# Kernel tuning notes

Hardware: AMD Instinct MI355X
Metric: run time of the kernel (lower is better)

Reference implementation:

```python
import jax, jax.numpy as jnp
import numpy as np

T, B, C, H, W = 4, 8, 256, 56, 56
HEADS = 8
D_NORM = 8.0
LAMDA = 1
CV = C * LAMDA
EPS = 1e-5


def quant_if(x, D):
    # Q_IFNode with Quant surrogate: integer spike counts clip(round(x),0,D),
    # straight-through gradient = 1 on [0, D].
    y = jnp.clip(jnp.round(x), 0.0, D)
    mask = ((x >= 0.0) & (x <= D)).astype(x.dtype)
    return x * mask + jax.lax.stop_gradient(y - x * mask)


def conv_bn(x, w, p):
    # 1x1 conv (pointwise channel mix) fused with eval-mode BatchNorm.
    # x: [T,B,Cin,H,W], w: [Cout,Cin], p: [4,Cout]=(gamma,beta,mean,var)
    y = jnp.einsum('oc,tbchw->tbohw', w, x)
    gamma, beta, mean, var = p[0], p[1], p[2], p[3]
    s = gamma / jnp.sqrt(var + EPS)
    return y * s[None, None, :, None, None] + (beta - mean * s)[None, None, :, None, None]


def _to_heads(t, c):
    # [T,B,c,H,W] -> [T,B,HEADS,N,c//HEADS]  (channel split h-outer, matches torch reshape)
    return t.reshape(T, B, HEADS, c // HEADS, H * W).transpose(0, 1, 2, 4, 3)


def setup_inputs():
    key = jax.random.key(0)
    ks = jax.random.split(key, 9)

    def bn_params(k, c):
        k1, k2, k3, k4 = jax.random.split(k, 4)
        return jnp.stack([
            jax.random.uniform(k1, (c,)) + 0.5,        # gamma
            jax.random.normal(k2, (c,)) * 0.1,          # beta
            jax.random.normal(k3, (c,)) * 0.1,          # running mean
            jax.random.uniform(k4, (c,)) + 0.5,         # running var
        ]).astype(jnp.float32)

    x = jax.random.normal(ks[0], (T, B, C, H, W), dtype=jnp.float32)
    w_scale = 1.0 / np.sqrt(C)
    return {
        'x': x,
        'qw': jax.random.normal(ks[1], (C, C), dtype=jnp.float32) * w_scale,
        'qbn': bn_params(ks[2], C),
        'kw': jax.random.normal(ks[3], (C, C), dtype=jnp.float32) * w_scale,
        'kbn': bn_params(ks[4], C),
        'vw': jax.random.normal(ks[5], (CV, C), dtype=jnp.float32) * w_scale,
        'vbn': bn_params(ks[6], CV),
        'pw': jax.random.normal(ks[7], (C, CV), dtype=jnp.float32) * w_scale,
        'pbn': bn_params(ks[8], C),
    }


def reference(x, qw, qbn, kw, kbn, vw, vbn, pw, pbn):
    dh = C // HEADS
    scale = dh ** (-0.5)

    xs = quant_if(x, D_NORM) / D_NORM                       # head_spike / D_Norm
    q = conv_bn(xs, qw, qbn)
    k = conv_bn(xs, kw, kbn)
    v = conv_bn(xs, vw, vbn)

    qh = _to_heads(quant_if(q, D_NORM) / D_NORM, C)         # [T,B,h,N,dh]
    kh = _to_heads(quant_if(k, D_NORM) / D_NORM, C)
    vh = _to_heads(quant_if(v, D_NORM) / D_NORM, CV)        # [T,B,h,N,dv]

    # Softmax-free linear attention: (q @ k^T) @ v == q @ (k^T @ v), O(N*d^2).
    kv = jnp.einsum('tbhnd,tbhne->tbhde', kh, vh)            # [T,B,h,dh,dv]
    o = jnp.einsum('tbhnd,tbhde->tbhne', qh, kv) * (scale * 2.0)

    # [T,B,h,N,dv] -> [T,B,CV,N]
    o = o.transpose(0, 1, 2, 4, 3).reshape(T, B, CV, H * W)
    o = quant_if(o, D_NORM) / D_NORM                         # attn_spike / D_Norm
    o = o.reshape(T, B, CV, H, W)
    out = conv_bn(o, pw, pbn)                                # [T,B,C,H,W]
    return out
```

## Files before the change

### kernel.cpp

```cpp
#include <hip/hip_runtime.h>
#include <stdint.h>

#define TB_ 32
#define C_ 256
#define N_ 3136
#define TBC (C_ * N_)
#define ACT_SZ (TB_ * TBC)
#define XSB_TB 819200
#define PARTS 7
#define CHUNK 448

typedef __attribute__((ext_vector_type(8))) short bf16x8;
typedef __attribute__((ext_vector_type(4))) float f32x4;

__device__ __forceinline__ void glds16(const void* gp, void* lp) {
  __builtin_amdgcn_global_load_lds(
      (const __attribute__((address_space(1))) unsigned int*)gp,
      (__attribute__((address_space(3))) unsigned int*)lp, 16, 0, 0);
}

__device__ __forceinline__ unsigned short bf16rn(float f, float* val) {
  unsigned b = __float_as_uint(f);
  unsigned r = (b + 0x7fffu + ((b >> 16) & 1u)) >> 16;
  *val = __uint_as_float(r << 16);
  return (unsigned short)r;
}

__device__ __forceinline__ int dot4u(unsigned a, unsigned b, int c) {
  c += (int)(a & 255u)         * (int)(b & 255u);
  c += (int)((a >> 8) & 255u)  * (int)((b >> 8) & 255u);
  c += (int)((a >> 16) & 255u) * (int)((b >> 16) & 255u);
  c += (int)(a >> 24)          * (int)(b >> 24);
  return c;
}

__device__ __forceinline__ int dot4(unsigned a, unsigned b, int c) {
#if defined(__has_builtin)
#if __has_builtin(__builtin_amdgcn_sdot4)
  return __builtin_amdgcn_sdot4((int)a, (int)b, c, false);
#else
  return dot4u(a, b, c);
#endif
#else
  return dot4u(a, b, c);
#endif
}

__global__ __launch_bounds__(256) void prep_all(
    const float* __restrict__ qbn, const float* __restrict__ kbn,
    const float* __restrict__ vbn, const float* __restrict__ pbn,
    const float* __restrict__ qw, const float* __restrict__ kw,
    const float* __restrict__ vw, const float* __restrict__ pw,
    float* __restrict__ bnw, unsigned short* __restrict__ wsp,
    int* __restrict__ kvg) {
  const int bx = blockIdx.x;
  const int t = threadIdx.x;
  if (bx == 0) {
    const float* ps[4] = {qbn, kbn, vbn, pbn};
#pragma unroll
    for (int i = 0; i < 4; ++i) {
      const float* p = ps[i];
      float g = p[t], be = p[256 + t], mn = p[512 + t], vr = p[768 + t];
      float s = g / sqrtf(vr + 1e-5f);
      float b = __fsub_rn(be, __fmul_rn(mn, s));
      bnw[i * 512 + t] = s;
      bnw[i * 512 + 256 + t] = b;
    }
  } else if (bx <= 1024) {
    const float* Ws[4] = {qw, kw, vw, pw};
    int id = bx - 1, co = id & 255, m = id >> 8;
    float w = Ws[m][co * 256 + t];
    float h1, h2, h3r;
    unsigned short u1 = bf16rn(w, &h1);
    float r1 = __fsub_rn(w, h1);
    unsigned short u2 = bf16rn(r1, &h2);
    float r2 = __fsub_rn(r1, h2);
    unsigned short u3 = bf16rn(r2, &h3r);
    int rt = co >> 7, ks = t >> 5;
    int lane = (co & 15) + 16 * ((t >> 3) & 3);
    unsigned short us[3] = {u1, u2, u3};
#pragma unroll
    for (int sp = 0; sp < 3; ++sp) {
      size_t off = (size_t)((((m * 3 + sp) * 2 + rt) * 8 + ks)) * 4096 + lane * 8 + (t & 7);
      wsp[off] = us[sp];
    }
  } else {
    int tb = bx - 1025;
    int4* p = (int4*)(kvg + (size_t)tb * 8192);
    for (int i = t; i < 2048; i += 256) p[i] = make_int4(0, 0, 0, 0);
  }
}

__global__ __launch_bounds__(256) void quant_x_t(const float* __restrict__ x,
                                                 unsigned short* __restrict__ xsb) {
  __shared__ unsigned short s[64 * 68];
  const int t = threadIdx.x;
  const int n0 = blockIdx.x * 64;
  const int tb = blockIdx.y;
  const float* X = x + (size_t)tb * TBC;
  const int nl = t & 63, cq = t >> 6;
  const int c16 = t >> 4, p4 = (t & 15) * 4;

  unsigned short* dstb = xsb + (size_t)tb * XSB_TB;
  for (int cb = 0; cb < 4; ++cb) {
    int cbase = cb * 64;
#pragma unroll
    for (int i = 0; i < 4; ++i) {
      int c = i * 16 + c16;
      float4 v = *(const float4*)&X[(size_t)(cbase + c) * N_ + n0 + p4];
      unsigned short r0 = (unsigned short)(__float_as_uint(fminf(fmaxf(rintf(v.x), 0.f), 8.f)) >> 16);
      unsigned short r1 = (unsigned short)(__float_as_uint(fminf(fmaxf(rintf(v.y), 0.f), 8.f)) >> 16);
      unsigned short r2 = (unsigned short)(__float_as_uint(fminf(fmaxf(rintf(v.z), 0.f), 8.f)) >> 16);
      unsigned short r3 = (unsigned short)(__float_as_uint(fminf(fmaxf(rintf(v.w), 0.f), 8.f)) >> 16);
      uint2 pk2;
      pk2.x = (unsigned)r0 | ((unsigned)r1 << 16);
      pk2.y = (unsigned)r2 | ((unsigned)r3 << 16);
      *(uint2*)&s[c * 68 + p4] = pk2;
    }
    __syncthreads();
#pragma unroll 2
    for (int j = 0; j < 2; ++j) {
      int ccl = j * 4 + cq;
      int cc = cb * 8 + ccl;
      unsigned short v8[8];
#pragma unroll
      for (int d = 0; d < 8; ++d) v8[d] = s[(ccl * 8 + d) * 68 + nl];
      int n = n0 + nl;
      uint4 pk;
      pk.x = (unsigned)v8[0] | ((unsigned)v8[1] << 16);
      pk.y = (unsigned)v8[2] | ((unsigned)v8[3] << 16);
      pk.z = (unsigned)v8[4] | ((unsigned)v8[5] << 16);
      pk.w = (unsigned)v8[6] | ((unsigned)v8[7] << 16);
      *(uint4*)&dstb[(size_t)(n >> 4) * 4096 + cc * 128 + (n & 15) * 8] = pk;
    }
    __syncthreads();
  }
}

__global__ __launch_bounds__(256) void qkv_mfma_sw(
    const unsigned short* __restrict__ xsb, const unsigned short* __restrict__ wsp,
    const float* __restrict__ bnw,
    uint8_t* __restrict__ qsb, uint8_t* __restrict__ ks_, uint8_t* __restrict__ vs) {
  __shared__ __align__(16) char smem[49152];
  const int t = threadIdx.x;
  const int L = t & 63, w = t >> 6;
  const int wrow = w >> 1, wcol = w & 1;
  const int b = blockIdx.x;
  const int oct = b / 48, rem = b % 48;
  const int s = rem >> 3, gl = rem & 7;
  const int g = oct * 8 + gl;
  const int ntile = g % 25, tb = g / 25;
  const int conv = s >> 1, rt = s & 1;
  const int n0 = ntile * 128;

  const char* Bb = (const char*)(xsb + (size_t)tb * XSB_TB) + (size_t)ntile * 65536;
  const char* Ab = (const char*)wsp + ((size_t)(conv * 3) * 16 + rt * 8) * 8192;

  f32x4 acc[4][4];
#pragma unroll
  for (int i = 0; i < 4; ++i)
#pragma unroll
    for (int j = 0; j < 4; ++j) acc[i][j] = (f32x4){0.f, 0.f, 0.f, 0.f};

  glds16(Ab + t * 16, smem + t * 16);
  glds16(Ab + t * 16 + 4096, smem + t * 16 + 4096);
  glds16(Bb + (size_t)w * 8192 + L * 16, smem + 8192 + t * 16);
  glds16(Bb + (size_t)(w + 4) * 8192 + L * 16, smem + 8192 + t * 16 + 4096);
  {
    char* slot1 = smem + 16384;
    const char* Ak1 = Ab + 8192;
    glds16(Ak1 + t * 16, slot1 + t * 16);
    glds16(Ak1 + t * 16 + 4096, slot1 + t * 16 + 4096);
    const char* Bk1 = Bb + 1024;
    glds16(Bk1 + (size_t)w * 8192 + L * 16, slot1 + 8192 + t * 16);
    glds16(Bk1 + (size_t)(w + 4) * 8192 + L * 16, slot1 + 8192 + t * 16 + 4096);
  }

#pragma unroll 1
  for (int st = 0; st < 24; ++st) {
    if (st < 23) {
      asm volatile("s_waitcnt vmcnt(4)" ::: "memory");
    } else {
      asm volatile("s_waitcnt vmcnt(0)" ::: "memory");
    }
    __builtin_amdgcn_s_barrier();
    const int s2 = st + 2;
    if (s2 < 24) {
      char* slotn = smem + (s2 % 3) * 16384;
      const char* Ak = Ab + (size_t)(((s2 >> 3) * 16) + (s2 & 7)) * 8192;
      glds16(Ak + t * 16, slotn + t * 16);
      glds16(Ak + t * 16 + 4096, slotn + t * 16 + 4096);
      const char* Bk = Bb + (size_t)(s2 & 7) * 1024;
      glds16(Bk + (size_t)w * 8192 + L * 16, slotn + 8192 + t * 16);
      glds16(Bk + (size_t)(w + 4) * 8192 + L * 16, slotn + 8192 + t * 16 + 4096);
    }
    char* slotc = smem + (st % 3) * 16384;
    bf16x8 af[4], bfr[4];
#pragma unroll
    for (int i = 0; i < 4; ++i) {
      af[i] = *(const bf16x8*)(slotc + (wrow * 4 + i) * 1024 + L * 16);
      bfr[i] = *(const bf16x8*)(slotc + 8192 + (wcol * 4 + i) * 1024 + L * 16);
    }
#pragma unroll
    for (int i = 0; i < 4; ++i)
#pragma unroll
      for (int j = 0; j < 4; ++j)
        acc[i][j] = __builtin_amdgcn_mfma_f32_16x16x32_bf16(af[i], bfr[j], acc[i][j], 0, 0, 0);
  }

  const float* sbn = bnw + conv * 512;
  const int rbase = rt * 128;
  if (conv == 0) {
    uint8_t* qtb = qsb + (size_t)tb * XSB_TB;
#pragma unroll
    for (int i = 0; i < 4; ++i) {
      int co0 = rbase + wrow * 64 + i * 16 + ((L >> 4) << 2);
      float s0 = sbn[co0], b0 = sbn[256 + co0];
      float s1 = sbn[co0 + 1], b1 = sbn[256 + co0 + 1];
      float s2v = sbn[co0 + 2], b2 = sbn[256 + co0 + 2];
      float s3 = sbn[co0 + 3], b3 = sbn[256 + co0 + 3];
#pragma unroll
      for (int j = 0; j < 4; ++j) {
        int n = n0 + wcol * 64 + j * 16 + (L & 15);
        if (n < N_) {
          float ss[4] = {s0, s1, s2v, s3}, bb[4] = {b0, b1, b2, b3};
          unsigned wb = 0;
#pragma unroll
          for (int r = 0; r < 4; ++r) {
            float y = acc[i][j][r] * 0.125f;
            float tt = __fadd_rn(__fmul_rn(y, ss[r]), bb[r]);
            float rr = fminf(fmaxf(rintf(tt), 0.f), 8.f);
            wb |= ((unsigned)(uint8_t)rr) << (8 * r);
          }
          *(unsigned*)&qtb[(size_t)(n >> 4) * 4096 + (co0 >> 3) * 128 + (n & 15) * 8 + (co0 & 7)] = wb;
        }
      }
    }
  } else {
    uint8_t* outp = (conv == 1 ? ks_ : vs) + (size_t)tb * TBC;
#pragma unroll
    for (int i = 0; i < 4; ++i) {
      int co0 = rbase + wrow * 64 + i * 16 + ((L >> 4) << 2);
#pragma unroll
      for (int j = 0; j < 4; ++j) {
        int n = n0 + wcol * 64 + j * 16 + (L & 15);
        if (n < N_) {
#pragma unroll
          for (int r = 0; r < 4; ++r) {
            int co = co0 + r;
            float y = acc[i][j][r] * 0.125f;
            float tt = __fadd_rn(__fmul_rn(y, sbn[co]), sbn[256 + co]);
            float rr = fminf(fmaxf(rintf(tt), 0.f), 8.f);
            outp[(size_t)co * N_ + n] = (uint8_t)rr;
          }
        }
      }
    }
  }
}

__global__ __launch_bounds__(256) void attn_kv(
    const uint8_t* __restrict__ ks, const uint8_t* __restrict__ vs,
    int* __restrict__ kvg) {
  const int h = blockIdx.x, tb = blockIdx.y, part = blockIdx.z;
  const int tid = threadIdx.x;
  __shared__ unsigned sk[32][68];
  __shared__ unsigned sv[32][68];
  const uint8_t* K = ks + (size_t)tb * TBC + h * 32 * N_;
  const uint8_t* V = vs + (size_t)tb * TBC + h * 32 * N_;
  const int d0 = (tid >> 4) * 2;
  const int e0 = (tid & 15) * 2;
  const int pbase = part * CHUNK;
  const int pend = pbase + CHUNK;
  int acc[2][2] = {};

  for (int nt = 0; nt < 2; ++nt) {
    int n0 = pbase + nt * 256;
    if (n0 >= pend) break;
    if (nt) __syncthreads();
#pragma unroll
    for (int i = 0; i < 8; ++i) {
      int idx = tid + i * 256;
      int d = idx >> 6, w2 = idx & 63;
      int n = n0 + w2 * 4;
      unsigned kw_ = 0, vw_ = 0;
      if (n < pend) {
        kw_ = *(const unsigned*)&K[d * N_ + n];
        vw_ = *(const unsigned*)&V[d * N_ + n];
      }
      sk[d][w2] = kw_;
      sv[d][w2] = vw_;
    }
    __syncthreads();
#pragma unroll
    for (int w2 = 0; w2 < 64; w2 += 4) {
      uint4 ka = *(const uint4*)&sk[d0][w2];
      uint4 kb = *(const uint4*)&sk[d0 + 1][w2];
      uint4 va = *(const uint4*)&sv[e0][w2];
      uint4 vb = *(const uint4*)&sv[e0 + 1][w2];
      unsigned kwds[2][4] = {{ka.x, ka.y, ka.z, ka.w}, {kb.x, kb.y, kb.z, kb.w}};
      unsigned vwds[2][4] = {{va.x, va.y, va.z, va.w}, {vb.x, vb.y, vb.z, vb.w}};
#pragma unroll
      for (int di = 0; di < 2; ++di)
#pragma unroll
        for (int ej = 0; ej < 2; ++ej)
#pragma unroll
          for (int c = 0; c < 4; ++c)
            acc[di][ej] = dot4(kwds[di][c], vwds[ej][c], acc[di][ej]);
    }
  }
  int* dst = kvg + ((size_t)(tb * 8 + h)) * 1024;
  atomicAdd(&dst[d0 * 32 + e0], acc[0][0]);
  atomicAdd(&dst[d0 * 32 + e0 + 1], acc[0][1]);
  atomicAdd(&dst[(d0 + 1) * 32 + e0], acc[1][0]);
  atomicAdd(&dst[(d0 + 1) * 32 + e0 + 1], acc[1][1]);
}

__global__ __launch_bounds__(256) void kv_finish(const int* __restrict__ kvg,
                                                 unsigned short* __restrict__ kvimg) {
  const int tb = blockIdx.x, t = threadIdx.x;
  const int* src = kvg + (size_t)tb * 8192;
  unsigned short* dst = kvimg + (size_t)tb * 24576;
#pragma unroll 4
  for (int i = 0; i < 32; ++i) {
    int idx = t + i * 256;
    int h = idx >> 10, rem = idx & 1023, d = rem >> 5, e = rem & 31;
    int v = src[idx];
    int b1 = (v > 0) ? (32 - __clz(v)) : 0;
    int sh1 = b1 > 8 ? b1 - 8 : 0;
    int hi = (v >> sh1) << sh1;
    int r1 = v - hi;
    int b2 = (r1 > 0) ? (32 - __clz(r1)) : 0;
    int sh2 = b2 > 8 ? b2 - 8 : 0;
    int mid = (r1 >> sh2) << sh2;
    int r2 = r1 - mid;
    int parts[3] = {hi, mid, r2};
    int mtile = e >> 4, lane = (e & 15) + 16 * (d >> 3), j = d & 7;
#pragma unroll
    for (int sp = 0; sp < 3; ++sp) {
      float f = (float)parts[sp];
      dst[(size_t)h * 3072 + (sp * 2 + mtile) * 512 + lane * 8 + j] =
          (unsigned short)(__float_as_uint(f) >> 16);
    }
  }
}

__global__ __launch_bounds__(256) void attn_o_mfma(
    const uint8_t* __restrict__ qsb, const unsigned short* __restrict__ kvimg,
    unsigned short* __restrict__ osb) {
  __shared__ __align__(16) char smem[14336];
  char* smB = smem;
  char* smA = smem + 8192;
  const int t = threadIdx.x;
  const int L = t & 63, wv = t >> 6;
  const int b = blockIdx.x;
  const int ntile = b % 25, tb = b / 25;
  const uint8_t* Q = qsb + (size_t)tb * XSB_TB + (size_t)ntile * 8 * 4096;
  const unsigned short* KV = kvimg + (size_t)tb * 24576;
  unsigned short* osb_tb = osb + (size_t)tb * XSB_TB;
  const float cscale = (float)(0.3535533905932738 / 512.0);

#pragma unroll 1
  for (int h = 0; h < 8; ++h) {
    __syncthreads();
    const char* Ah = (const char*)(KV + (size_t)h * 3072);
    glds16(Ah + t * 16, smA + t * 16);
    if (t < 128) glds16(Ah + 4096 + t * 16, smA + 4096 + t * 16);
#pragma unroll
    for (int it = 0; it < 4; ++it) {
      int w2 = t + it * 256;
      int gl2 = w2 >> 7;
      int wl = w2 & 127;
      int ccp = wl >> 5;
      int rem = (w2 * 4) & 127;
      int n16 = rem >> 3, k7b = rem & 7;
      unsigned wd = *(const unsigned*)&Q[(size_t)gl2 * 4096 + (h * 4 + ccp) * 128 + n16 * 8 + k7b];
      unsigned short* ds = (unsigned short*)smB + gl2 * 512 + (ccp * 16 + n16) * 8 + k7b;
      float f0 = (float)(wd & 255u), f1 = (float)((wd >> 8) & 255u);
      float f2 = (float)((wd >> 16) & 255u), f3 = (float)(wd >> 24);
      uint2 pk;
      pk.x = (__float_as_uint(f0) >> 16) | ((__float_as_uint(f1) >> 16) << 16);
      pk.y = (__float_as_uint(f2) >> 16) | ((__float_as_uint(f3) >> 16) << 16);
      *(uint2*)ds = pk;
    }
    __syncthreads();
    bf16x8 bfr[2];
#pragma unroll
    for (int jj = 0; jj < 2; ++jj)
      bfr[jj] = *(const bf16x8*)(smB + (wv * 2 + jj) * 1024 + L * 16);
    f32x4 acc[2][2];
#pragma unroll
    for (int i = 0; i < 2; ++i)
#pragma unroll
      for (int jj = 0; jj < 2; ++jj) acc[i][jj] = (f32x4){0.f, 0.f, 0.f, 0.f};
#pragma unroll
    for (int sp = 0; sp < 3; ++sp) {
      bf16x8 a0 = *(const bf16x8*)(smA + (sp * 2 + 0) * 1024 + L * 16);
      bf16x8 a1 = *(const bf16x8*)(smA + (sp * 2 + 1) * 1024 + L * 16);
#pragma unroll
      for (int jj = 0; jj < 2; ++jj) {
        acc[0][jj] = __builtin_amdgcn_mfma_f32_16x16x32_bf16(a0, bfr[jj], acc[0][jj], 0, 0, 0);
        acc[1][jj] = __builtin_amdgcn_mfma_f32_16x16x32_bf16(a1, bfr[jj], acc[1][jj], 0, 0, 0);
      }
    }
#pragma unroll
    for (int i = 0; i < 2; ++i) {
      int c0 = h * 32 + i * 16 + ((L >> 4) << 2);
#pragma unroll
      for (int jj = 0; jj < 2; ++jj) {
        int n = ntile * 128 + (wv * 2 + jj) * 16 + (L & 15);
        if (n < N_) {
          unsigned short u[4];
#pragma unroll
          for (int r = 0; r < 4; ++r) {
            float of = acc[i][jj][r] * cscale;
            float rr = fminf(fmaxf(rintf(of), 0.f), 8.f);
            u[r] = (unsigned short)(__float_as_uint(rr) >> 16);
          }
          uint2 pk;
          pk.x = (unsigned)u[0] | ((unsigned)u[1] << 16);
          pk.y = (unsigned)u[2] | ((unsigned)u[3] << 16);
          *(uint2*)&osb_tb[(size_t)(n >> 4) * 4096 + (c0 >> 3) * 128 + (n & 15) * 8 + (c0 & 7)] = pk;
        }
      }
    }
  }
}

__global__ __launch_bounds__(256) void out_mfma_sw(
    const unsigned short* __restrict__ osb, const unsigned short* __restrict__ wsp,
    const float* __restrict__ bnw, float* __restrict__ out) {
  __shared__ __align__(16) char smem[49152];
  const int t = threadIdx.x;
  const int L = t & 63, w = t >> 6;
  const int wrow = w >> 1, wcol = w & 1;
  const int b = blockIdx.x;
  const int oct = b / 16, rem = b % 16;
  const int rt = rem >> 3, gl = rem & 7;
  const int g = oct * 8 + gl;
  const int ntile = g % 25, tb = g / 25;
  const int n0 = ntile * 128;
  const char* Bb = (const char*)(osb + (size_t)tb * XSB_TB) + (size_t)ntile * 65536;
  const char* Ab = (const char*)wsp + ((size_t)9 * 16 + rt * 8) * 8192;

  f32x4 acc[4][4];
#pragma unroll
  for (int i = 0; i < 4; ++i)
#pragma unroll
    for (int j = 0; j < 4; ++j) acc[i][j] = (f32x4){0.f, 0.f, 0.f, 0.f};

  glds16(Ab + t * 16, smem + t * 16);
  glds16(Ab + t * 16 + 4096, smem + t * 16 + 4096);
  glds16(Bb + (size_t)w * 8192 + L * 16, smem + 8192 + t * 16);
  glds16(Bb + (size_t)(w + 4) * 8192 + L * 16, smem + 8192 + t * 16 + 4096);
  {
    char* slot1 = smem + 16384;
    const char* Ak1 = Ab + 8192;
    glds16(Ak1 + t * 16, slot1 + t * 16);
    glds16(Ak1 + t * 16 + 4096, slot1 + t * 16 + 4096);
    const char* Bk1 = Bb + 1024;
    glds16(Bk1 + (size_t)w * 8192 + L * 16, slot1 + 8192 + t * 16);
    glds16(Bk1 + (size_t)(w + 4) * 8192 + L * 16, slot1 + 8192 + t * 16 + 4096);
  }

#pragma unroll 1
  for (int st = 0; st < 16; ++st) {
    if (st < 15) {
      asm volatile("s_waitcnt vmcnt(4)" ::: "memory");
    } else {
      asm volatile("s_waitcnt vmcnt(0)" ::: "memory");
    }
    __builtin_amdgcn_s_barrier();
    const int s2 = st + 2;
    if (s2 < 16) {
      char* slotn = smem + (s2 % 3) * 16384;
      const char* Ak = Ab + (size_t)(((s2 >> 3) * 16) + (s2 & 7)) * 8192;
      glds16(Ak + t * 16, slotn + t * 16);
      glds16(Ak + t * 16 + 4096, slotn + t * 16 + 4096);
      const char* Bk = Bb + (size_t)(s2 & 7) * 1024;
      glds16(Bk + (size_t)w * 8192 + L * 16, slotn + 8192 + t * 16);
      glds16(Bk + (size_t)(w + 4) * 8192 + L * 16, slotn + 8192 + t * 16 + 4096);
    }
    char* slotc = smem + (st % 3) * 16384;
    bf16x8 af[4], bfr[4];
#pragma unroll
    for (int i = 0; i < 4; ++i) {
      af[i] = *(const bf16x8*)(slotc + (wrow * 4 + i) * 1024 + L * 16);
      bfr[i] = *(const bf16x8*)(slotc + 8192 + (wcol * 4 + i) * 1024 + L * 16);
    }
#pragma unroll
    for (int i = 0; i < 4; ++i)
#pragma unroll
      for (int j = 0; j < 4; ++j)
        acc[i][j] = __builtin_amdgcn_mfma_f32_16x16x32_bf16(af[i], bfr[j], acc[i][j], 0, 0, 0);
  }

  float* O = out + (size_t)tb * TBC;
  const float* sbn = bnw + 3 * 512;
  const int rbase = rt * 128;
#pragma unroll
  for (int i = 0; i < 4; ++i) {
    int co0 = rbase + wrow * 64 + i * 16 + ((L >> 4) << 2);
#pragma unroll
    for (int j = 0; j < 4; ++j) {
      int n = n0 + wcol * 64 + j * 16 + (L & 15);
      if (n < N_) {
#pragma unroll
        for (int r = 0; r < 4; ++r) {
          int co = co0 + r;
          float y = acc[i][j][r] * 0.125f;
          O[(size_t)co * N_ + n] = __fadd_rn(__fmul_rn(y, sbn[co]), sbn[256 + co]);
        }
      }
    }
  }
}

extern "C" void kernel_launch(void* const* d_in, const int* in_sizes, int n_in,
                              void* d_out, int out_size, void* d_ws, size_t ws_size,
                              hipStream_t stream) {
  const float* x   = (const float*)d_in[0];
  const float* qw  = (const float*)d_in[1];
  const float* qbn = (const float*)d_in[2];
  const float* kw  = (const float*)d_in[3];
  const float* kbn = (const float*)d_in[4];
  const float* vw  = (const float*)d_in[5];
  const float* vbn = (const float*)d_in[6];
  const float* pw  = (const float*)d_in[7];
  const float* pbn = (const float*)d_in[8];
  float* out = (float*)d_out;

  uint8_t* ws = (uint8_t*)d_ws;
  float* bnw           = (float*)ws;
  unsigned short* wsp  = (unsigned short*)(ws + 8192);
  unsigned short* xsb  = (unsigned short*)(ws + 1581056);
  uint8_t* qsb         = ws + 54009856;
  uint8_t* ksp         = ws + 80224256;
  uint8_t* vsp         = ws + 105914368;
  int* kvg             = (int*)(ws + 131604480);
  unsigned short* kvimg = (unsigned short*)(ws + 132653056);
  unsigned short* osb  = xsb;

  prep_all<<<1057, 256, 0, stream>>>(qbn, kbn, vbn, pbn, qw, kw, vw, pw, bnw, wsp, kvg);
  quant_x_t<<<dim3(49, 32), 256, 0, stream>>>(x, xsb);
  qkv_mfma_sw<<<4800, 256, 0, stream>>>(xsb, wsp, bnw, qsb, ksp, vsp);
  attn_kv<<<dim3(8, 32, PARTS), 256, 0, stream>>>(ksp, vsp, kvg);
  kv_finish<<<32, 256, 0, stream>>>(kvg, kvimg);
  attn_o_mfma<<<800, 256, 0, stream>>>(qsb, kvimg, osb);
  out_mfma_sw<<<1600, 256, 0, stream>>>(osb, wsp, bnw, out);
}
```

Measured before the change: 397.0 us.

## Double-buffer per-head loads in attn_o and swizzle V LDS layout in attn_kv

The attn_o_mfma kernel now uses two LDS buffers. It prefetches the next head's KV image via global_load_lds and loads the next head's Q spikes into registers while the current head's MFMAs run, then converts and stores them afterwards. This overlaps global load latency with compute, at the cost of doubling shared memory per block, which may lower occupancy. Separately, attn_kv XOR-swizzles the V tile columns in LDS to reduce bank conflicts on the uint4 reads.

Result: no change. 395.8 us (-0.3%).

```diff
diff --git a/kernel.cpp b/kernel.cpp
--- a/kernel.cpp
+++ b/kernel.cpp
@@ -270,6 +270,7 @@
   const uint8_t* V = vs + (size_t)tb * TBC + h * 32 * N_;
   const int d0 = (tid >> 4) * 2;
   const int e0 = (tid & 15) * 2;
+  const int vsw = ((e0 >> 1) & 7) << 2;
   const int pbase = part * CHUNK;
   const int pend = pbase + CHUNK;
   int acc[2][2] = {};
@@ -289,15 +290,15 @@
         vw_ = *(const unsigned*)&V[d * N_ + n];
       }
       sk[d][w2] = kw_;
-      sv[d][w2] = vw_;
+      sv[d][w2 ^ (((d >> 1) & 7) << 2)] = vw_;
     }
     __syncthreads();
 #pragma unroll
     for (int w2 = 0; w2 < 64; w2 += 4) {
       uint4 ka = *(const uint4*)&sk[d0][w2];
       uint4 kb = *(const uint4*)&sk[d0 + 1][w2];
-      uint4 va = *(const uint4*)&sv[e0][w2];
-      uint4 vb = *(const uint4*)&sv[e0 + 1][w2];
+      uint4 va = *(const uint4*)&sv[e0][w2 ^ vsw];
+      uint4 vb = *(const uint4*)&sv[e0 + 1][w2 ^ vsw];
       unsigned kwds[2][4] = {{ka.x, ka.y, ka.z, ka.w}, {kb.x, kb.y, kb.z, kb.w}};
       unsigned vwds[2][4] = {{va.x, va.y, va.z, va.w}, {vb.x, vb.y, vb.z, vb.w}};
 #pragma unroll
@@ -348,9 +349,7 @@
 __global__ __launch_bounds__(256) void attn_o_mfma(
     const uint8_t* __restrict__ qsb, const unsigned short* __restrict__ kvimg,
     unsigned short* __restrict__ osb) {
-  __shared__ __align__(16) char smem[14336];
-  char* smB = smem;
-  char* smA = smem + 8192;
+  __shared__ __align__(16) char smem[28672];
   const int t = threadIdx.x;
   const int L = t & 63, wv = t >> 6;
   const int b = blockIdx.x;
@@ -360,21 +359,19 @@
   unsigned short* osb_tb = osb + (size_t)tb * XSB_TB;
   const float cscale = (float)(0.3535533905932738 / 512.0);
 
-#pragma unroll 1
-  for (int h = 0; h < 8; ++h) {
-    __syncthreads();
-    const char* Ah = (const char*)(KV + (size_t)h * 3072);
+  const int gl2_[4] = {t >> 7, (t + 256) >> 7, (t + 512) >> 7, (t + 768) >> 7};
+  {
+    char* smB = smem;
+    char* smA = smem + 8192;
+    const char* Ah = (const char*)KV;
     glds16(Ah + t * 16, smA + t * 16);
     if (t < 128) glds16(Ah + 4096 + t * 16, smA + 4096 + t * 16);
 #pragma unroll
     for (int it = 0; it < 4; ++it) {
       int w2 = t + it * 256;
-      int gl2 = w2 >> 7;
-      int wl = w2 & 127;
-      int ccp = wl >> 5;
-      int rem = (w2 * 4) & 127;
-      int n16 = rem >> 3, k7b = rem & 7;
-      unsigned wd = *(const unsigned*)&Q[(size_t)gl2 * 4096 + (h * 4 + ccp) * 128 + n16 * 8 + k7b];
+      int gl2 = w2 >> 7, wl = w2 & 127, ccp = wl >> 5;
+      int rem = (w2 * 4) & 127, n16 = rem >> 3, k7b = rem & 7;
+      unsigned wd = *(const unsigned*)&Q[(size_t)gl2 * 4096 + (0 * 4 + ccp) * 128 + n16 * 8 + k7b];
       unsigned short* ds = (unsigned short*)smB + gl2 * 512 + (ccp * 16 + n16) * 8 + k7b;
       float f0 = (float)(wd & 255u), f1 = (float)((wd >> 8) & 255u);
       float f2 = (float)((wd >> 16) & 255u), f3 = (float)(wd >> 24);
@@ -383,11 +380,32 @@
       pk.y = (__float_as_uint(f2) >> 16) | ((__float_as_uint(f3) >> 16) << 16);
       *(uint2*)ds = pk;
     }
+  }
+
+#pragma unroll 1
+  for (int h = 0; h < 8; ++h) {
     __syncthreads();
+    char* cur = smem + (h & 1) * 14336;
+    char* smB = cur;
+    char* smA = cur + 8192;
     bf16x8 bfr[2];
 #pragma unroll
     for (int jj = 0; jj < 2; ++jj)
       bfr[jj] = *(const bf16x8*)(smB + (wv * 2 + jj) * 1024 + L * 16);
+    unsigned wd[4];
+    if (h < 7) {
+      char* alt = smem + ((h + 1) & 1) * 14336;
+      const char* Ah = (const char*)(KV + (size_t)(h + 1) * 3072);
+      glds16(Ah + t * 16, alt + 8192 + t * 16);
+      if (t < 128) glds16(Ah + 4096 + t * 16, alt + 8192 + 4096 + t * 16);
+#pragma unroll
+      for (int it = 0; it < 4; ++it) {
+        int w2 = t + it * 256;
+        int gl2 = w2 >> 7, wl = w2 & 127, ccp = wl >> 5;
+        int rem = (w2 * 4) & 127, n16 = rem >> 3, k7b = rem & 7;
+        wd[it] = *(const unsigned*)&Q[(size_t)gl2 * 4096 + ((h + 1) * 4 + ccp) * 128 + n16 * 8 + k7b];
+      }
+    }
     f32x4 acc[2][2];
 #pragma unroll
     for (int i = 0; i < 2; ++i)
@@ -401,6 +419,22 @@
       for (int jj = 0; jj < 2; ++jj) {
         acc[0][jj] = __builtin_amdgcn_mfma_f32_16x16x32_bf16(a0, bfr[jj], acc[0][jj], 0, 0, 0);
         acc[1][jj] = __builtin_amdgcn_mfma_f32_16x16x32_bf16(a1, bfr[jj], acc[1][jj], 0, 0, 0);
+      }
+    }
+    if (h < 7) {
+      char* alt = smem + ((h + 1) & 1) * 14336;
+#pragma unroll
+      for (int it = 0; it < 4; ++it) {
+        int w2 = t + it * 256;
+        int gl2 = w2 >> 7, wl = w2 & 127, ccp = wl >> 5;
+        int rem = (w2 * 4) & 127, n16 = rem >> 3, k7b = rem & 7;
+        unsigned short* ds = (unsigned short*)alt + gl2 * 512 + (ccp * 16 + n16) * 8 + k7b;
+        float f0 = (float)(wd[it] & 255u), f1 = (float)((wd[it] >> 8) & 255u);
+        float f2 = (float)((wd[it] >> 16) & 255u), f3 = (float)(wd[it] >> 24);
+        uint2 pk;
+        pk.x = (__float_as_uint(f0) >> 16) | ((__float_as_uint(f1) >> 16) << 16);
+        pk.y = (__float_as_uint(f2) >> 16) | ((__float_as_uint(f3) >> 16) << 16);
+        *(uint2*)ds = pk;
       }
     }
 #pragma unroll
```
